# Kernel tuning notes

Hardware: AMD Instinct MI355X
Metric: run time of the kernel (lower is better)

## Reference

```python
import jax, jax.numpy as jnp
import numpy as np

W = 0.5
EM_ITER = 5
SCALE = 20.0
N, T, D_IN, D_OUT, K, C1 = 16, 750, 2048, 2048, 8, 21  # C1 = class_num + 1


def l2n(f):
    # torch.norm(p=2, dim=-1, keepdim=True); divide with 1e-9 eps
    return f / (jnp.linalg.norm(f, axis=-1, keepdims=True) + 1e-9)


def setup_inputs() -> dict:
    key = jax.random.key(0)
    ks = jax.random.split(key, 5)
    x = jax.random.normal(ks[0], (N, T, D_IN), dtype=jnp.float32)
    W_emb = jax.random.normal(ks[1], (D_IN, D_OUT), dtype=jnp.float32) * (1.0 / np.sqrt(D_IN))
    b_emb = jnp.zeros((D_OUT,), dtype=jnp.float32)
    mu_param = jax.random.normal(ks[2], (K, D_OUT), dtype=jnp.float32) * 0.02
    ac_center = jax.random.normal(ks[3], (C1, D_OUT), dtype=jnp.float32) * 0.02
    fg_center = -1.0 * ac_center[-1][None, :]
    return {"x": x, "W_emb": W_emb, "b_emb": b_emb, "mu_param": mu_param,
            "ac_center": ac_center, "fg_center": fg_center}


def em(mu, x):
    norm_x = l2n(x)
    for _ in range(EM_ITER):
        norm_mu = l2n(mu)
        z = jax.nn.softmax(jnp.einsum('nkd,ntd->nkt', norm_mu, norm_x) * 5.0, axis=1)
        nz = z / (jnp.sum(z, axis=-1, keepdims=True) + 1e-9)
        mu = jnp.einsum('nkt,ntd->nkd', nz, x)
    return mu


def random_walk(x, y, w):
    n, t, _ = x.shape
    x_n, y_n = l2n(x), l2n(y)
    z = jax.nn.softmax(jnp.einsum('nkd,ntd->nkt', y_n, x_n) * 5.0, axis=1)  # (n,k,t)
    nz = z / (jnp.sum(z, axis=-1, keepdims=True) + 1e-9)
    affinity = jnp.einsum('nkt,nks->nts', z, nz)                             # (n,t,t)
    eye_t = jnp.eye(t, dtype=x.dtype)
    y2x_sum_x = w * jnp.einsum('nkt,nkd->ntd', z, y) + x
    # (I - w^2 A)^{-1} @ y2x_sum_x, expressed as a batched solve (same math as torch.solve)
    refined = (1.0 - w) * jnp.linalg.solve(eye_t[None] - (w * w) * affinity, y2x_sum_x)
    return refined


def prediction_module(x, ac_center, fg_center):
    nx = l2n(x)
    nac = l2n(ac_center)
    nfg = l2n(fg_center)
    frm_scrs = jnp.einsum('ntd,cd->ntc', nx, nac) * SCALE        # (n,t,C1)
    frm_fb = jnp.einsum('ntd,kd->ntk', nx, nfg)[..., 0] * SCALE  # (n,t)
    ca_att = jax.nn.sigmoid(frm_fb)
    cw_att = jax.nn.sigmoid(frm_scrs)
    ca_natt = ca_att / (jnp.sum(ca_att, axis=1, keepdims=True) + 1e-5)
    cw_natt = cw_att / (jnp.sum(cw_att, axis=1, keepdims=True) + 1e-5)
    ca_feat = jnp.einsum('ntd,nt->nd', x, ca_natt)
    cw_feat = jnp.einsum('ntd,ntc->ncd', x, cw_natt)
    ca_scr = jnp.einsum('nd,cd->nc', l2n(ca_feat), nac) * SCALE
    cw_scr = jnp.einsum('ncd,cd->nc', l2n(cw_feat), nac) * SCALE
    return (jax.nn.softmax(ca_scr, axis=-1), jax.nn.softmax(cw_scr, axis=-1), ca_att, frm_scrs)


def forward(x, W_emb, b_emb, mu_param, ac_center, fg_center):
    n = x.shape[0]
    x = jax.nn.relu(x @ W_emb + b_emb)  # feature_embedding (Dropout is identity in eval)
    mu = jnp.broadcast_to(mu_param[None], (n,) + mu_param.shape)
    mu = em(mu, x)
    reallocated_x = random_walk(x, mu, W)
    o_ca, o_cw, o_att, o_frm = prediction_module(x, ac_center, fg_center)
    m_ca, m_cw, m_att, m_frm = prediction_module(reallocated_x, ac_center, fg_center)
    mu_scr = jnp.einsum('nkd,cd->nkc', l2n(mu), l2n(ac_center)) * SCALE
    mu_pred = jax.nn.softmax(mu_scr, axis=-1)
    return (o_ca, o_cw, o_att, o_frm, m_ca, m_cw, m_att, m_frm, x, mu, mu_pred)


def reference(x, W_emb, b_emb, mu_param, ac_center, fg_center):
    return forward(x, W_emb, b_emb, mu_param, ac_center, fg_center)
```

## Files before the change

kernel.cpp:

```cpp
#include <hip/hip_runtime.h>

#define NB 16
#define TT 750
#define DD 2048
#define KK 8
#define CC 21
#define NT 12000

#define MU_CH 16
#define MU_TCH 47

typedef __bf16 bf16;
typedef __attribute__((ext_vector_type(4))) float floatx4;
typedef __attribute__((ext_vector_type(8))) __bf16 bf16x8;
typedef __attribute__((ext_vector_type(4))) __bf16 bf16x4;

__device__ __forceinline__ float wave_allreduce_sum(float v) {
#pragma unroll
  for (int m = 32; m > 0; m >>= 1) v += __shfl_xor(v, m, 64);
  return v;
}

__device__ __forceinline__ void async_lds16(const bf16* g, bf16* l) {
  __builtin_amdgcn_global_load_lds(
      (const __attribute__((address_space(1))) void*)(g),
      (__attribute__((address_space(3))) void*)(l), 16, 0, 0);
}

__global__ __launch_bounds__(256) void k_prep(
    const float* __restrict__ W, bf16* __restrict__ Wt,
    const float* __restrict__ ac, const float* __restrict__ fg,
    float* __restrict__ nacf, bf16* __restrict__ nacb,
    const float* __restrict__ mup, float* __restrict__ nmu, bf16* __restrict__ nmub,
    const float* __restrict__ x, bf16* __restrict__ Ab) {
  int b = blockIdx.x, tid = threadIdx.x;
  __shared__ float tile[32][33];
  __shared__ float sb[4];
  if (b < 4096) {
    int j0 = (b & 63) * 32, k0 = (b >> 6) * 32;
    int tx = tid & 31, ty = tid >> 5;
#pragma unroll
    for (int i = 0; i < 4; i++)
      tile[ty + 8 * i][tx] = W[(size_t)(k0 + ty + 8 * i) * DD + j0 + tx];
    __syncthreads();
#pragma unroll
    for (int i = 0; i < 4; i++)
      Wt[(size_t)(j0 + ty + 8 * i) * DD + k0 + tx] = (bf16)tile[tx][ty + 8 * i];
    return;
  }
  if (b < 4128) {
    int r = b - 4096;
    int d0 = tid * 8;
    if (r >= 22) {
#pragma unroll
      for (int j = 0; j < 8; j++) nacb[(size_t)r * DD + d0 + j] = (bf16)0.f;
      return;
    }
    const float* src = (r < 21) ? (ac + (size_t)r * DD) : fg;
    float v[8];
    floatx4 a = *(const floatx4*)(src + d0);
    floatx4 c = *(const floatx4*)(src + d0 + 4);
    v[0]=a.x; v[1]=a.y; v[2]=a.z; v[3]=a.w; v[4]=c.x; v[5]=c.y; v[6]=c.z; v[7]=c.w;
    float ss = 0.f;
#pragma unroll
    for (int j = 0; j < 8; j++) ss += v[j] * v[j];
    ss = wave_allreduce_sum(ss);
    int lane = tid & 63, wid = tid >> 6;
    if (lane == 0) sb[wid] = ss;
    __syncthreads();
    float inv = 1.f / (sqrtf(sb[0] + sb[1] + sb[2] + sb[3]) + 1e-9f);
#pragma unroll
    for (int j = 0; j < 8; j++) {
      float nv = v[j] * inv;
      nacf[(size_t)r * DD + d0 + j] = nv;
      nacb[(size_t)r * DD + d0 + j] = (bf16)nv;
    }
    return;
  }
  if (b < 4256) {
    int bb = b - 4128;
    int n = bb >> 3, k = bb & 7;
    int lane = tid & 63, wid = tid >> 6;
    const float* p = mup + (size_t)k * DD + tid * 8;
    float v[8];
    floatx4 a = *(const floatx4*)p;
    floatx4 c = *(const floatx4*)(p + 4);
    v[0]=a.x; v[1]=a.y; v[2]=a.z; v[3]=a.w; v[4]=c.x; v[5]=c.y; v[6]=c.z; v[7]=c.w;
    float ss = 0.f;
#pragma unroll
    for (int j = 0; j < 8; j++) ss += v[j] * v[j];
    ss = wave_allreduce_sum(ss);
    if (lane == 0) sb[wid] = ss;
    __syncthreads();
    float inv = 1.f / (sqrtf(sb[0] + sb[1] + sb[2] + sb[3]) + 1e-9f);
    float* q = nmu + (size_t)bb * DD + tid * 8;
    bf16* qb = nmub + (size_t)(n * 16 + k) * DD + tid * 8;
#pragma unroll
    for (int j = 0; j < 8; j++) {
      float nv = v[j] * inv;
      q[j] = nv;
      qb[j] = (bf16)nv;
    }
    return;
  }
  int unit0 = (b - 4256) * 4;
#pragma unroll
  for (int u = 0; u < 4; u++) {
    size_t base = ((size_t)(unit0 + u) * 256 + tid) * 8;
    int row = (int)(base >> 11);
    bf16x8 o = {};
    if (row < NT) {
      floatx4 a = *(const floatx4*)(x + base);
      floatx4 c = *(const floatx4*)(x + base + 4);
      o[0]=(bf16)a.x; o[1]=(bf16)a.y; o[2]=(bf16)a.z; o[3]=(bf16)a.w;
      o[4]=(bf16)c.x; o[5]=(bf16)c.y; o[6]=(bf16)c.z; o[7]=(bf16)c.w;
    }
    *(bf16x8*)(Ab + base) = o;
  }
}

__global__ __launch_bounds__(256) void k_gemm(
    const bf16* __restrict__ Ab, const bf16* __restrict__ Bt,
    const float* __restrict__ bias,
    float* __restrict__ Cout, bf16* __restrict__ Cb, float* __restrict__ rowsq) {
  __shared__ bf16 As[128 * 64];
  __shared__ bf16 Bs[128 * 64];
  int tid = threadIdx.x;
  int bid = blockIdx.x;
  int xcd = bid & 7;
  int j = bid >> 3;
  int n0 = (xcd * 2 + (j >= 94 ? 1 : 0)) * 128;
  int m0 = (j % 94) * 128;
  int wid = tid >> 6, lane = tid & 63;
  int wm = (wid >> 1) * 64, wn = (wid & 1) * 64;
  int lrow = lane & 15, lko = (lane >> 4) * 8;
  int lr7 = lrow & 7;
  floatx4 acc[4][4] = {};
  int crow = tid >> 3;
  int jg = ((tid & 7) ^ (crow & 7)) * 8;
  const bf16* gA = Ab + (size_t)(m0 + crow) * DD + jg;
  const bf16* gB = Bt + (size_t)(n0 + crow) * DD + jg;
  bf16* lA = As + tid * 8;
  bf16* lB = Bs + tid * 8;
  for (int k0 = 0; k0 < DD; k0 += 64) {
#pragma unroll
    for (int s = 0; s < 4; s++)
      async_lds16(gA + (size_t)(32 * s) * DD + k0, lA + 2048 * s);
#pragma unroll
    for (int s = 0; s < 4; s++)
      async_lds16(gB + (size_t)(32 * s) * DD + k0, lB + 2048 * s);
    __syncthreads();
#pragma unroll
    for (int ks = 0; ks < 64; ks += 32) {
      bf16x8 af[4], bfr[4];
#pragma unroll
      for (int i = 0; i < 4; i++) {
        int sw = (((ks + lko) >> 3) ^ lr7) * 8;
        af[i] = *(const bf16x8*)(As + (wm + i * 16 + lrow) * 64 + sw);
      }
#pragma unroll
      for (int jj = 0; jj < 4; jj++) {
        int sw = (((ks + lko) >> 3) ^ lr7) * 8;
        bfr[jj] = *(const bf16x8*)(Bs + (wn + jj * 16 + lrow) * 64 + sw);
      }
#pragma unroll
      for (int i = 0; i < 4; i++)
#pragma unroll
        for (int jj = 0; jj < 4; jj++)
          acc[i][jj] = __builtin_amdgcn_mfma_f32_16x16x32_bf16(af[i], bfr[jj], acc[i][jj], 0, 0, 0);
    }
    __syncthreads();
  }
  int quad = lane >> 4;
  float bv[4];
#pragma unroll
  for (int jj = 0; jj < 4; jj++) bv[jj] = bias[n0 + wn + jj * 16 + lrow];
#pragma unroll
  for (int i = 0; i < 4; i++) {
#pragma unroll
    for (int r = 0; r < 4; r++) {
      int row = m0 + wm + i * 16 + quad * 4 + r;
      bool ok = (row < NT);
      float sq = 0.f;
#pragma unroll
      for (int jj = 0; jj < 4; jj++) {
        int col = n0 + wn + jj * 16 + lrow;
        float v = acc[i][jj][r] + bv[jj];
        v = fmaxf(v, 0.f);
        if (ok) {
          Cout[(size_t)row * DD + col] = v;
          Cb[(size_t)row * DD + col] = (bf16)v;
        }
        sq += v * v;
      }
#pragma unroll
      for (int m = 1; m < 16; m <<= 1) sq += __shfl_xor(sq, m, 64);
      if (ok && lrow == 0) atomicAdd(&rowsq[row], sq);
    }
  }
}

__global__ __launch_bounds__(256) void k_score(
    const bf16* __restrict__ Xb, const bf16* __restrict__ nmub,
    const float* __restrict__ rowsq,
    float* __restrict__ z, float* __restrict__ rowsum) {
  __shared__ bf16 As[2][64 * 64];
  __shared__ bf16 Bs[2][16 * 64];
  int tid = threadIdx.x, lane = tid & 63, w = tid >> 6;
  int m0 = blockIdx.x * 64, n = blockIdx.y;
  int lrow = lane & 15, lko = (lane >> 4) * 8, lr7 = lrow & 7;
  int crow = tid >> 3;
  int jg = ((tid & 7) ^ (crow & 7)) * 8;
  const bf16* gA = Xb + (size_t)(n * TT + m0 + crow) * DD + jg;
  const bf16* gB = nmub + (size_t)(n * 16 + (crow & 15)) * DD + jg;
  async_lds16(gA, &As[0][tid * 8]);
  async_lds16(gA + (size_t)32 * DD, &As[0][2048 + tid * 8]);
  if (tid < 128) async_lds16(gB, &Bs[0][tid * 8]);
  floatx4 acc = {};
  int buf = 0;
  for (int k0 = 0; k0 < DD; k0 += 64) {
    __syncthreads();
    if (k0 + 64 < DD) {
      async_lds16(gA + k0 + 64, &As[buf ^ 1][tid * 8]);
      async_lds16(gA + (size_t)32 * DD + k0 + 64, &As[buf ^ 1][2048 + tid * 8]);
      if (tid < 128) async_lds16(gB + k0 + 64, &Bs[buf ^ 1][tid * 8]);
    }
#pragma unroll
    for (int ks = 0; ks < 64; ks += 32) {
      int sw = ((((ks + lko) >> 3)) ^ lr7) * 8;
      bf16x8 a = *(const bf16x8*)(&As[buf][(w * 16 + lrow) * 64 + sw]);
      bf16x8 b = *(const bf16x8*)(&Bs[buf][lrow * 64 + sw]);
      acc = __builtin_amdgcn_mfma_f32_16x16x32_bf16(a, b, acc, 0, 0, 0);
    }
    buf ^= 1;
  }
  int quad = lane >> 4;
  int k = lrow;
  float pacc = 0.f;
#pragma unroll
  for (int r = 0; r < 4; r++) {
    int trow = m0 + w * 16 + quad * 4 + r;
    bool valid = (trow < TT);
    float rq = valid ? rowsq[n * TT + trow] : 1.f;
    float s = acc[r] * (5.f / (sqrtf(rq) + 1e-9f));
    float mx = s;
    mx = fmaxf(mx, __shfl_xor(mx, 1, 64));
    mx = fmaxf(mx, __shfl_xor(mx, 2, 64));
    mx = fmaxf(mx, __shfl_xor(mx, 4, 64));
    float e = __expf(s - mx);
    float se = e;
    se += __shfl_xor(se, 1, 64);
    se += __shfl_xor(se, 2, 64);
    se += __shfl_xor(se, 4, 64);
    float zz = e / se;
    zz = (valid && k < 8) ? zz : 0.f;
    if (valid && k < 8) z[(size_t)(n * TT + trow) * 8 + k] = zz;
    pacc += zz;
  }
  pacc += __shfl_xor(pacc, 16, 64);
  pacc += __shfl_xor(pacc, 32, 64);
  if (lane < 8) atomicAdd(&rowsum[n * 8 + lane], pacc);
}

__global__ __launch_bounds__(256) void k_mu_accum(
    const bf16* __restrict__ Xb, const float* __restrict__ z,
    float* __restrict__ part2) {
  int n = blockIdx.x, tc = blockIdx.y, tid = threadIdx.x;
  int t0 = tc * MU_TCH;
  int tcnt = min(MU_TCH, TT - t0);
  __shared__ float zs[MU_TCH * 8];
  for (int i = tid; i < tcnt * 8; i += 256) zs[i] = z[(size_t)(n * TT + t0) * 8 + i];
  __syncthreads();
  float acc[8][8] = {};
  const bf16* xp = Xb + (size_t)(n * TT + t0) * DD + tid * 8;
  bf16x8 x0 = *(const bf16x8*)xp;
  bf16x8 x1 = (tcnt > 1) ? *(const bf16x8*)(xp + DD) : x0;
  for (int tt = 0; tt < tcnt; tt++) {
    bf16x8 cur = x0;
    x0 = x1;
    if (tt + 2 < tcnt) x1 = *(const bf16x8*)(xp + (size_t)(tt + 2) * DD);
    float xv[8];
#pragma unroll
    for (int j = 0; j < 8; j++) xv[j] = (float)cur[j];
    floatx4 za = *(const floatx4*)&zs[tt * 8];
    floatx4 zb4 = *(const floatx4*)&zs[tt * 8 + 4];
    float zk[8] = {za.x, za.y, za.z, za.w, zb4.x, zb4.y, zb4.z, zb4.w};
#pragma unroll
    for (int k = 0; k < 8; k++)
#pragma unroll
      for (int j = 0; j < 8; j++) acc[k][j] += zk[k] * xv[j];
  }
  float* pb = part2 + ((size_t)(tc * 16 + n) * 8) * DD + tid * 8;
#pragma unroll
  for (int k = 0; k < 8; k++) {
    floatx4 lo = {acc[k][0], acc[k][1], acc[k][2], acc[k][3]};
    floatx4 hi = {acc[k][4], acc[k][5], acc[k][6], acc[k][7]};
    *(floatx4*)(pb + (size_t)k * DD) = lo;
    *(floatx4*)(pb + (size_t)k * DD + 4) = hi;
  }
}

__global__ void k_mu_finish(const float* __restrict__ part2, const float* __restrict__ rs,
                            float* __restrict__ accS_raw, float* __restrict__ mu_ws,
                            float* __restrict__ mu_out, float* __restrict__ nmu_out,
                            bf16* __restrict__ nmub) {
  int b = blockIdx.x;
  int n = b >> 3, k = b & 7;
  int tid = threadIdx.x, lane = tid & 63, wid = tid >> 6;
  int d0 = tid * 8;
  float s[8] = {};
#pragma unroll 4
  for (int c = 0; c < MU_CH; c++) {
    const float* p = part2 + ((size_t)(c * 16 + n) * 8 + k) * DD + d0;
    floatx4 a = *(const floatx4*)p;
    floatx4 cc = *(const floatx4*)(p + 4);
    s[0] += a.x; s[1] += a.y; s[2] += a.z; s[3] += a.w;
    s[4] += cc.x; s[5] += cc.y; s[6] += cc.z; s[7] += cc.w;
  }
  if (accS_raw != nullptr) {
#pragma unroll
    for (int j = 0; j < 8; j++) accS_raw[(size_t)b * DD + d0 + j] = s[j];
    return;
  }
  float invr = 1.f / (rs[b] + 1e-9f);
  float m[8];
#pragma unroll
  for (int j = 0; j < 8; j++) m[j] = s[j] * invr;
#pragma unroll
  for (int j = 0; j < 8; j++) mu_ws[(size_t)b * DD + d0 + j] = m[j];
  if (mu_out != nullptr) {
#pragma unroll
    for (int j = 0; j < 8; j++) mu_out[(size_t)b * DD + d0 + j] = m[j];
  }
  float ss = 0.f;
#pragma unroll
  for (int j = 0; j < 8; j++) ss += m[j] * m[j];
  ss = wave_allreduce_sum(ss);
  __shared__ float sb[4];
  if (lane == 0) sb[wid] = ss;
  __syncthreads();
  float inv = 1.f / (sqrtf(sb[0] + sb[1] + sb[2] + sb[3]) + 1e-9f);
  bf16* qb = nmub + (size_t)(n * 16 + k) * DD + d0;
#pragma unroll
  for (int j = 0; j < 8; j++) {
    float nv = m[j] * inv;
    nmu_out[(size_t)b * DD + d0 + j] = nv;
    qb[j] = (bf16)nv;
  }
}

__global__ void k_wood_mupred(const float* __restrict__ z, const float* __restrict__ rowsum,
                              const float* __restrict__ S, const float* __restrict__ mu,
                              float* __restrict__ G,
                              const float* __restrict__ nmu, const float* __restrict__ nacf,
                              float* __restrict__ mupred) {
  int tid = threadIdx.x;
  if (blockIdx.x >= 16) {
    int b = blockIdx.x - 16;
    int lane = tid & 63, wid = tid >> 6;
    const float* v = nmu + (size_t)b * DD;
    __shared__ float scr[21];
    for (int c = wid; c < 21; c += 4) {
      const float* a = nacf + (size_t)c * DD;
      float s = 0.f;
      for (int i = lane * 4; i < DD; i += 256) {
        floatx4 vv = *(const floatx4*)(v + i);
        floatx4 aa = *(const floatx4*)(a + i);
        s += vv.x * aa.x + vv.y * aa.y + vv.z * aa.z + vv.w * aa.w;
      }
      s = wave_allreduce_sum(s);
      if (lane == 0) scr[c] = s * 20.f;
    }
    __syncthreads();
    if (tid == 0) {
      float mx = scr[0];
      for (int c = 1; c < 21; c++) mx = fmaxf(mx, scr[c]);
      float se = 0.f;
      for (int c = 0; c < 21; c++) se += __expf(scr[c] - mx);
      float inv = 1.f / se;
      for (int c = 0; c < 21; c++) mupred[(size_t)b * 21 + c] = __expf(scr[c] - mx) * inv;
    }
    return;
  }
  int n = blockIdx.x;
  __shared__ float VU[8][8];
  __shared__ float Mi[8][8];
  __shared__ float invrs[8];
  __shared__ float vus[64][4];
  if (tid < 8) invrs[tid] = 1.f / (rowsum[n * 8 + tid] + 1e-9f);
  {
    int pr = tid >> 2, sl = tid & 3;
    int jj = pr >> 3, kk = pr & 7;
    float s = 0.f;
    for (int t = sl; t < TT; t += 4) {
      const float* zp = z + (size_t)(n * TT + t) * 8;
      s += zp[jj] * zp[kk];
    }
    vus[pr][sl] = s;
  }
  __syncthreads();
  if (tid < 64)
    VU[tid >> 3][tid & 7] =
        (vus[tid][0] + vus[tid][1] + vus[tid][2] + vus[tid][3]) * invrs[tid >> 3];
  __syncthreads();
  if (tid == 0) {
    float M[8][16];
    for (int i = 0; i < 8; i++)
      for (int jj = 0; jj < 8; jj++) {
        M[i][jj] = ((i == jj) ? 1.f : 0.f) - 0.25f * VU[i][jj];
        M[i][8 + jj] = (i == jj) ? 1.f : 0.f;
      }
    for (int c = 0; c < 8; c++) {
      float pv = 1.f / M[c][c];
      for (int jj = 0; jj < 16; jj++) M[c][jj] *= pv;
      for (int rr = 0; rr < 8; rr++)
        if (rr != c) {
          float f = M[rr][c];
          for (int jj = 0; jj < 16; jj++) M[rr][jj] -= f * M[c][jj];
        }
    }
    for (int i = 0; i < 8; i++)
      for (int jj = 0; jj < 8; jj++) Mi[i][jj] = M[i][8 + jj];
  }
  __syncthreads();
  const float* mun = mu + (size_t)n * 8 * DD;
  const float* Sn = S + (size_t)n * 8 * DD;
  float* Gn = G + (size_t)n * 8 * DD;
  for (int d = tid; d < DD; d += 256) {
    float m[8], P[8];
#pragma unroll
    for (int k = 0; k < 8; k++) m[k] = mun[k * DD + d];
#pragma unroll
    for (int k = 0; k < 8; k++) {
      float s = 0.f;
#pragma unroll
      for (int jj = 0; jj < 8; jj++) s += VU[k][jj] * m[jj];
      P[k] = 0.5f * s + Sn[k * DD + d] * invrs[k];
    }
#pragma unroll
    for (int jj = 0; jj < 8; jj++) {
      float s = 0.f;
#pragma unroll
      for (int k = 0; k < 8; k++) s += Mi[jj][k] * P[k];
      Gn[jj * DD + d] = 0.5f * (0.5f * m[jj] + 0.25f * s);
    }
  }
}

__global__ __launch_bounds__(256) void k_rw_passC(
    const bf16* __restrict__ Xb, const float* __restrict__ z,
    const float* __restrict__ G, bf16* __restrict__ refb,
    float* __restrict__ invr) {
  int n = blockIdx.x, ch = blockIdx.y, tid = threadIdx.x;
  int lane = tid & 63, wid = tid >> 6;
  int d0 = tid * 8;
  int t0 = ch * 30;
  const float* Gn = G + (size_t)n * 8 * DD;
  float gr[8][8];
#pragma unroll
  for (int k = 0; k < 8; k++) {
    floatx4 a = *(const floatx4*)(Gn + k * DD + d0);
    floatx4 b = *(const floatx4*)(Gn + k * DD + d0 + 4);
    gr[k][0]=a.x; gr[k][1]=a.y; gr[k][2]=a.z; gr[k][3]=a.w;
    gr[k][4]=b.x; gr[k][5]=b.y; gr[k][6]=b.z; gr[k][7]=b.w;
  }
  __shared__ float red[30][4];
  const bf16* xrow = Xb + (size_t)n * TT * DD;
  bf16x8 xg = *(const bf16x8*)(xrow + (size_t)t0 * DD + d0);
  for (int tt = 0; tt < 30; tt++) {
    int t = t0 + tt;
    bf16x8 x8 = xg;
    if (tt + 1 < 30) xg = *(const bf16x8*)(xrow + (size_t)(t + 1) * DD + d0);
    const float* zp = z + (size_t)(n * TT + t) * 8;
    floatx4 za = *(const floatx4*)zp;
    floatx4 zb4 = *(const floatx4*)(zp + 4);
    float zt[8] = {za.x, za.y, za.z, za.w, zb4.x, zb4.y, zb4.z, zb4.w};
    float r[8];
#pragma unroll
    for (int j = 0; j < 8; j++) {
      float s = 0.5f * (float)x8[j];
#pragma unroll
      for (int k = 0; k < 8; k++) s += zt[k] * gr[k][j];
      r[j] = s;
    }
    bf16x8 ro;
#pragma unroll
    for (int j = 0; j < 8; j++) ro[j] = (bf16)r[j];
    *(bf16x8*)(refb + (size_t)(n * TT + t) * DD + d0) = ro;
    float ss = 0.f;
#pragma unroll
    for (int j = 0; j < 8; j++) ss += r[j] * r[j];
    ss = wave_allreduce_sum(ss);
    if (lane == 0) red[tt][wid] = ss;
  }
  __syncthreads();
  if (tid < 30) {
    float tot = red[tid][0] + red[tid][1] + red[tid][2] + red[tid][3];
    invr[n * TT + t0 + tid] = 1.f / (sqrtf(tot) + 1e-9f);
  }
}

__global__ __launch_bounds__(256) void k_pred_p1(
    const bf16* __restrict__ Xb, const bf16* __restrict__ nacb,
    const float* __restrict__ invn, int mode,
    float* __restrict__ out_frm, float* __restrict__ out_att,
    float* __restrict__ natt, float* __restrict__ att_sums) {
  __shared__ bf16 As[2][2048];
  __shared__ bf16 Bs[2][2048];
  __shared__ float ssum[2][32];
  int tid = threadIdx.x, lane = tid & 63, wid = tid >> 6;
  int m0 = blockIdx.x * 32;
  if (tid < 64) ssum[tid >> 5][tid & 31] = 0.f;
  int lrow = lane & 15, lko = (lane >> 4) * 8;
  int lr7 = lrow & 7;
  int r0 = (wid & 1) * 16, c0 = (wid >> 1) * 16;
  int crow = tid >> 3;
  int jg = ((tid & 7) ^ (crow & 7)) * 8;
  const bf16* gA = Xb + (size_t)(m0 + crow) * DD + jg;
  const bf16* gB = nacb + (size_t)crow * DD + jg;
  async_lds16(gA, &As[0][tid * 8]);
  async_lds16(gB, &Bs[0][tid * 8]);
  floatx4 acc = {};
  int buf = 0;
  for (int k0 = 0; k0 < DD; k0 += 64) {
    __syncthreads();
    if (k0 + 64 < DD) {
      async_lds16(gA + k0 + 64, &As[buf ^ 1][tid * 8]);
      async_lds16(gB + k0 + 64, &Bs[buf ^ 1][tid * 8]);
    }
#pragma unroll
    for (int ks = 0; ks < 64; ks += 32) {
      int sw = ((((ks + lko) >> 3) ^ lr7)) * 8;
      bf16x8 a = *(const bf16x8*)(&As[buf][(r0 + lrow) * 64 + sw]);
      bf16x8 b = *(const bf16x8*)(&Bs[buf][(c0 + lrow) * 64 + sw]);
      acc = __builtin_amdgcn_mfma_f32_16x16x32_bf16(a, b, acc, 0, 0, 0);
    }
    buf ^= 1;
  }
  __syncthreads();
  int quad = lane >> 4;
  int nbase = m0 / TT;
  int c = c0 + lrow;
#pragma unroll
  for (int r = 0; r < 4; r++) {
    int row = m0 + r0 + quad * 4 + r;
    if (c < 22) {
      float iv = mode ? (1.f / (sqrtf(invn[row]) + 1e-9f)) : invn[row];
      float s = acc[r] * iv * 20.f;
      float sg = 1.f / (1.f + __expf(-s));
      int n_loc = row / TT - nbase;
      if (c < 21) out_frm[(size_t)row * 21 + c] = s;
      else out_att[row] = sg;
      natt[(size_t)row * 22 + c] = sg;
      atomicAdd(&ssum[n_loc][c], sg);
    }
  }
  __syncthreads();
  if (tid < 64) {
    int nl = tid >> 5, cs = tid & 31;
    int nn = nbase + nl;
    if (cs < 22 && nn < NB) {
      float v = ssum[nl][cs];
      if (v != 0.f) atomicAdd(&att_sums[nn * 22 + cs], v);
    }
  }
}

__global__ __launch_bounds__(256) void k_pred_p2(
    const bf16* __restrict__ Xb, const float* __restrict__ natt,
    const float* __restrict__ sums, float* __restrict__ partF) {
  int n = blockIdx.x, dh = blockIdx.y, tc = blockIdx.z, tid = threadIdx.x;
  int d = dh * 1024 + tid * 4;
  int t0 = tc * 94;
  int tcnt = min(94, TT - t0);
  __shared__ float sw[94 * 22];
  for (int i = tid; i < tcnt * 22; i += 256) {
    int c = i - (i / 22) * 22;
    sw[i] = natt[(size_t)(n * TT + t0) * 22 + i] / (sums[n * 22 + c] + 1e-5f);
  }
  __syncthreads();
  float ac[22][4] = {};
  const bf16* xrow = Xb + (size_t)n * TT * DD;
  bf16x4 xg = *(const bf16x4*)(xrow + (size_t)t0 * DD + d);
  for (int tt = 0; tt < tcnt; tt++) {
    bf16x4 x4 = xg;
    if (tt + 1 < tcnt) xg = *(const bf16x4*)(xrow + (size_t)(t0 + tt + 1) * DD + d);
    float xv[4] = {(float)x4[0], (float)x4[1], (float)x4[2], (float)x4[3]};
#pragma unroll
    for (int cidx = 0; cidx < 22; cidx++) {
      float w = sw[tt * 22 + cidx];
#pragma unroll
      for (int jj = 0; jj < 4; jj++) ac[cidx][jj] += w * xv[jj];
    }
  }
  float* pb = partF + ((size_t)(n * 8 + tc) * 22) * DD + d;
#pragma unroll
  for (int cidx = 0; cidx < 22; cidx++) {
    floatx4 v = {ac[cidx][0], ac[cidx][1], ac[cidx][2], ac[cidx][3]};
    *(floatx4*)(pb + (size_t)cidx * DD) = v;
  }
}

__global__ void k_feat_finish(const float* __restrict__ partF, float* __restrict__ feats) {
  int idx = blockIdx.x * 256 + threadIdx.x;
  if (idx >= NB * 22 * DD) return;
  int n = idx / (22 * DD);
  int rem = idx - n * (22 * DD);
  const float* p = partF + ((size_t)n * 8) * (22 * DD) + rem;
  float s = 0.f;
#pragma unroll
  for (int tc = 0; tc < 8; tc++) s += p[(size_t)tc * 22 * DD];
  feats[idx] = s;
}

__global__ void k_pred_final(const float* __restrict__ feats, const float* __restrict__ nacf,
                             float* __restrict__ oca, float* __restrict__ ocw) {
  int n = blockIdx.x, tid = threadIdx.x, lane = tid & 63, wid = tid >> 6;
  const float* fn = feats + (size_t)n * 22 * DD;
  __shared__ float rnorm[22];
  __shared__ float scr[42];
  for (int r = wid; r < 22; r += 4) {
    const float* fv = fn + (size_t)r * DD;
    float s = 0.f;
    for (int i = lane * 4; i < DD; i += 256) {
      floatx4 v = *(const floatx4*)(fv + i);
      s += v.x * v.x + v.y * v.y + v.z * v.z + v.w * v.w;
    }
    s = wave_allreduce_sum(s);
    if (lane == 0) rnorm[r] = 1.f / (sqrtf(s) + 1e-9f);
  }
  __syncthreads();
  for (int idx = wid; idx < 42; idx += 4) {
    int c = (idx < 21) ? idx : (idx - 21);
    int fr = (idx < 21) ? c : 21;
    const float* fv = fn + (size_t)fr * DD;
    const float* av = nacf + (size_t)c * DD;
    float s = 0.f;
    for (int i = lane * 4; i < DD; i += 256) {
      floatx4 v = *(const floatx4*)(fv + i);
      floatx4 a = *(const floatx4*)(av + i);
      s += v.x * a.x + v.y * a.y + v.z * a.z + v.w * a.w;
    }
    s = wave_allreduce_sum(s);
    if (lane == 0) scr[idx] = s * 20.f * rnorm[fr];
  }
  __syncthreads();
  if (tid < 2) {
    int base = (tid == 0) ? 21 : 0;
    float* dst = ((tid == 0) ? oca : ocw) + (size_t)n * 21;
    float mx = scr[base];
    for (int c = 1; c < 21; c++) mx = fmaxf(mx, scr[base + c]);
    float se = 0.f;
    for (int c = 0; c < 21; c++) se += __expf(scr[base + c] - mx);
    float inv = 1.f / se;
    for (int c = 0; c < 21; c++) dst[c] = __expf(scr[base + c] - mx) * inv;
  }
}

extern "C" void kernel_launch(void* const* d_in, const int* in_sizes, int n_in,
                              void* d_out, int out_size, void* d_ws, size_t ws_size,
                              hipStream_t stream) {
  const float* x_in = (const float*)d_in[0];
  const float* W = (const float*)d_in[1];
  const float* bemb = (const float*)d_in[2];
  const float* mup = (const float*)d_in[3];
  const float* ac = (const float*)d_in[4];
  const float* fg = (const float*)d_in[5];
  float* out = (float*)d_out;

  char* ws = (char*)d_ws;
  bf16* Wt = (bf16*)ws;
  bf16* Xb = (bf16*)(ws + 8388608);
  bf16* Rb = (bf16*)(ws + 57671680);
  bf16* Ab = (bf16*)(ws + 106954752);
  float* part2 = (float*)(ws + 106954752);
  float* partF = (float*)(ws + 106954752);
  bf16* nacb = (bf16*)(ws + 156237824);
  float* f = (float*)(ws + 156368896);
  float* nacf = f;
  float* mu = nacf + 45056;
  float* nmu = mu + 262144;
  bf16* nmub = (bf16*)(nmu + 262144);
  float* accS = nmu + 262144 + 262144;
  float* G = accS + 262144;
  float* z = G + 262144;
  float* natt = z + 96000;
  float* feats = natt + 264000;
  float* invr = feats + 720896;
  float* rowsum = invr + 12032;
  float* asums_o = rowsum + 768;
  float* asums_m = asums_o + 352;
  float* rowsq = asums_m + 352;

  float* o_ca = out;
  float* o_cw = out + 336;
  float* o_att = out + 672;
  float* o_frm = out + 12672;
  float* m_ca = out + 264672;
  float* m_cw = out + 265008;
  float* m_att = out + 265344;
  float* m_frm = out + 277344;
  float* x_out = out + 529344;
  float* mu_out = out + 25105344;
  float* mup_out = out + 25367488;

  hipMemsetAsync(rowsum, 0, (768 + 352 + 352 + 12032) * sizeof(float), stream);
  hipMemsetAsync(nmub, 0, (size_t)NB * 16 * DD * sizeof(bf16), stream);
  k_prep<<<7264, 256, 0, stream>>>(W, Wt, ac, fg, nacf, nacb, mup, nmu, nmub, x_in, Ab);
  k_gemm<<<1504, 256, 0, stream>>>(Ab, Wt, bemb, x_out, Xb, rowsq);
  for (int it = 0; it < 5; it++) {
    bool last = (it == 4);
    k_score<<<dim3(12, 16), 256, 0, stream>>>(Xb, nmub, rowsq, z, rowsum + it * 128);
    k_mu_accum<<<dim3(16, MU_CH), 256, 0, stream>>>(Xb, z, part2);
    k_mu_finish<<<128, 256, 0, stream>>>(part2, rowsum + it * 128, nullptr, mu,
                                         last ? mu_out : nullptr, nmu, nmub);
  }
  k_score<<<dim3(12, 16), 256, 0, stream>>>(Xb, nmub, rowsq, z, rowsum + 5 * 128);
  k_mu_accum<<<dim3(16, MU_CH), 256, 0, stream>>>(Xb, z, part2);
  k_mu_finish<<<128, 256, 0, stream>>>(part2, nullptr, accS, nullptr, nullptr, nullptr, nullptr);
  k_wood_mupred<<<144, 256, 0, stream>>>(z, rowsum + 5 * 128, accS, mu, G, nmu, nacf, mup_out);
  k_rw_passC<<<dim3(16, 25), 256, 0, stream>>>(Xb, z, G, Rb, invr);
  k_pred_p1<<<375, 256, 0, stream>>>(Xb, nacb, rowsq, 1, o_frm, o_att, natt, asums_o);
  k_pred_p2<<<dim3(16, 2, 8), 256, 0, stream>>>(Xb, natt, asums_o, partF);
  k_feat_finish<<<2816, 256, 0, stream>>>(partF, feats);
  k_pred_final<<<16, 256, 0, stream>>>(feats, nacf, o_ca, o_cw);
  k_pred_p1<<<375, 256, 0, stream>>>(Rb, nacb, invr, 0, m_frm, m_att, natt, asums_m);
  k_pred_p2<<<dim3(16, 2, 8), 256, 0, stream>>>(Rb, natt, asums_m, partF);
  k_feat_finish<<<2816, 256, 0, stream>>>(partF, feats);
  k_pred_final<<<16, 256, 0, stream>>>(feats, nacf, m_ca, m_cw);
}
```

Before: 915.9 us.

## Widen K-tile to 256 in score and pred GEMMs; fuse feat reduction into pred_final

The k_score and k_pred_p1 GEMM loops now stage 256-wide K slices in shared memory instead of 64, with a matching XOR swizzle. This cuts the number of barriers and loop iterations by four and issues more async loads per phase, at the cost of much larger LDS per block (about 80KB for k_score), which may lower occupancy. Separately, the k_feat_finish reduction over the 8 t-chunks is folded into k_pred_final, removing one launch per prediction pass. The cost is that this reduction now runs on only 16 blocks.

New measurement: 889.0 us. 1.03x faster.

```diff
diff --git a/kernel.cpp b/kernel.cpp
--- a/kernel.cpp
+++ b/kernel.cpp
@@ -204,32 +204,54 @@
     const bf16* __restrict__ Xb, const bf16* __restrict__ nmub,
     const float* __restrict__ rowsq,
     float* __restrict__ z, float* __restrict__ rowsum) {
-  __shared__ bf16 As[2][64 * 64];
-  __shared__ bf16 Bs[2][16 * 64];
+  __shared__ bf16 As[2][64 * 256];
+  __shared__ bf16 Bs[2][16 * 256];
   int tid = threadIdx.x, lane = tid & 63, w = tid >> 6;
   int m0 = blockIdx.x * 64, n = blockIdx.y;
   int lrow = lane & 15, lko = (lane >> 4) * 8, lr7 = lrow & 7;
-  int crow = tid >> 3;
-  int jg = ((tid & 7) ^ (crow & 7)) * 8;
-  const bf16* gA = Xb + (size_t)(n * TT + m0 + crow) * DD + jg;
-  const bf16* gB = nmub + (size_t)(n * 16 + (crow & 15)) * DD + jg;
-  async_lds16(gA, &As[0][tid * 8]);
-  async_lds16(gA + (size_t)32 * DD, &As[0][2048 + tid * 8]);
-  if (tid < 128) async_lds16(gB, &Bs[0][tid * 8]);
+  int scg = tid & 31;
+  int srow = tid >> 5;
+  const bf16* gXn = Xb + (size_t)(n * TT + m0) * DD;
+  const bf16* gBn = nmub + (size_t)(n * 16) * DD;
+#pragma unroll
+  for (int r = 0; r < 8; r++) {
+    int row = r * 8 + srow;
+    int cgg = (scg & 24) | ((scg & 7) ^ (row & 7));
+    async_lds16(gXn + (size_t)row * DD + cgg * 8, &As[0][r * 2048 + tid * 8]);
+  }
+#pragma unroll
+  for (int r = 0; r < 2; r++) {
+    int row = r * 8 + srow;
+    int cgg = (scg & 24) | ((scg & 7) ^ (row & 7));
+    async_lds16(gBn + (size_t)row * DD + cgg * 8, &Bs[0][r * 2048 + tid * 8]);
+  }
   floatx4 acc = {};
   int buf = 0;
-  for (int k0 = 0; k0 < DD; k0 += 64) {
+  for (int k0 = 0; k0 < DD; k0 += 256) {
     __syncthreads();
-    if (k0 + 64 < DD) {
-      async_lds16(gA + k0 + 64, &As[buf ^ 1][tid * 8]);
-      async_lds16(gA + (size_t)32 * DD + k0 + 64, &As[buf ^ 1][2048 + tid * 8]);
-      if (tid < 128) async_lds16(gB + k0 + 64, &Bs[buf ^ 1][tid * 8]);
-    }
-#pragma unroll
-    for (int ks = 0; ks < 64; ks += 32) {
-      int sw = ((((ks + lko) >> 3)) ^ lr7) * 8;
-      bf16x8 a = *(const bf16x8*)(&As[buf][(w * 16 + lrow) * 64 + sw]);
-      bf16x8 b = *(const bf16x8*)(&Bs[buf][lrow * 64 + sw]);
+    if (k0 + 256 < DD) {
+#pragma unroll
+      for (int r = 0; r < 8; r++) {
+        int row = r * 8 + srow;
+        int cgg = (scg & 24) | ((scg & 7) ^ (row & 7));
+        async_lds16(gXn + (size_t)row * DD + k0 + 256 + cgg * 8,
+                    &As[buf ^ 1][r * 2048 + tid * 8]);
+      }
+#pragma unroll
+      for (int r = 0; r < 2; r++) {
+        int row = r * 8 + srow;
+        int cgg = (scg & 24) | ((scg & 7) ^ (row & 7));
+        async_lds16(gBn + (size_t)row * DD + k0 + 256 + cgg * 8,
+                    &Bs[buf ^ 1][r * 2048 + tid * 8]);
+      }
+    }
+    int arow = w * 16 + lrow;
+#pragma unroll
+    for (int ks = 0; ks < 256; ks += 32) {
+      int cg = (ks + lko) >> 3;
+      int cgl = (cg & 24) | ((cg & 7) ^ lr7);
+      bf16x8 a = *(const bf16x8*)(&As[buf][arow * 256 + cgl * 8]);
+      bf16x8 b = *(const bf16x8*)(&Bs[buf][lrow * 256 + cgl * 8]);
       acc = __builtin_amdgcn_mfma_f32_16x16x32_bf16(a, b, acc, 0, 0, 0);
     }
     buf ^= 1;
@@ -505,34 +527,46 @@
     const float* __restrict__ invn, int mode,
     float* __restrict__ out_frm, float* __restrict__ out_att,
     float* __restrict__ natt, float* __restrict__ att_sums) {
-  __shared__ bf16 As[2][2048];
-  __shared__ bf16 Bs[2][2048];
+  __shared__ bf16 As[2][32 * 256];
+  __shared__ bf16 Bs[2][32 * 256];
   __shared__ float ssum[2][32];
   int tid = threadIdx.x, lane = tid & 63, wid = tid >> 6;
   int m0 = blockIdx.x * 32;
   if (tid < 64) ssum[tid >> 5][tid & 31] = 0.f;
-  int lrow = lane & 15, lko = (lane >> 4) * 8;
-  int lr7 = lrow & 7;
+  int lrow = lane & 15, lko = (lane >> 4) * 8, lr7 = lrow & 7;
   int r0 = (wid & 1) * 16, c0 = (wid >> 1) * 16;
-  int crow = tid >> 3;
-  int jg = ((tid & 7) ^ (crow & 7)) * 8;
-  const bf16* gA = Xb + (size_t)(m0 + crow) * DD + jg;
-  const bf16* gB = nacb + (size_t)crow * DD + jg;
-  async_lds16(gA, &As[0][tid * 8]);
-  async_lds16(gB, &Bs[0][tid * 8]);
+  int scg = tid & 31;
+  int srow = tid >> 5;
+  const bf16* gA = Xb + (size_t)m0 * DD;
+  const bf16* gB = nacb;
+#pragma unroll
+  for (int r = 0; r < 4; r++) {
+    int row = r * 8 + srow;
+    int cgg = (scg & 24) | ((scg & 7) ^ (row & 7));
+    async_lds16(gA + (size_t)row * DD + cgg * 8, &As[0][r * 2048 + tid * 8]);
+    async_lds16(gB + (size_t)row * DD + cgg * 8, &Bs[0][r * 2048 + tid * 8]);
+  }
   floatx4 acc = {};
   int buf = 0;
-  for (int k0 = 0; k0 < DD; k0 += 64) {
+  for (int k0 = 0; k0 < DD; k0 += 256) {
     __syncthreads();
-    if (k0 + 64 < DD) {
-      async_lds16(gA + k0 + 64, &As[buf ^ 1][tid * 8]);
-      async_lds16(gB + k0 + 64, &Bs[buf ^ 1][tid * 8]);
-    }
-#pragma unroll
-    for (int ks = 0; ks < 64; ks += 32) {
-      int sw = ((((ks + lko) >> 3) ^ lr7)) * 8;
-      bf16x8 a = *(const bf16x8*)(&As[buf][(r0 + lrow) * 64 + sw]);
-      bf16x8 b = *(const bf16x8*)(&Bs[buf][(c0 + lrow) * 64 + sw]);
+    if (k0 + 256 < DD) {
+#pragma unroll
+      for (int r = 0; r < 4; r++) {
+        int row = r * 8 + srow;
+        int cgg = (scg & 24) | ((scg & 7) ^ (row & 7));
+        async_lds16(gA + (size_t)row * DD + k0 + 256 + cgg * 8,
+                    &As[buf ^ 1][r * 2048 + tid * 8]);
+        async_lds16(gB + (size_t)row * DD + k0 + 256 + cgg * 8,
+                    &Bs[buf ^ 1][r * 2048 + tid * 8]);
+      }
+    }
+#pragma unroll
+    for (int ks = 0; ks < 256; ks += 32) {
+      int cg = (ks + lko) >> 3;
+      int cgl = (cg & 24) | ((cg & 7) ^ lr7);
+      bf16x8 a = *(const bf16x8*)(&As[buf][(r0 + lrow) * 256 + cgl * 8]);
+      bf16x8 b = *(const bf16x8*)(&Bs[buf][(c0 + lrow) * 256 + cgl * 8]);
       acc = __builtin_amdgcn_mfma_f32_16x16x32_bf16(a, b, acc, 0, 0, 0);
     }
     buf ^= 1;
@@ -601,22 +635,24 @@
   }
 }
 
-__global__ void k_feat_finish(const float* __restrict__ partF, float* __restrict__ feats) {
-  int idx = blockIdx.x * 256 + threadIdx.x;
-  if (idx >= NB * 22 * DD) return;
-  int n = idx / (22 * DD);
-  int rem = idx - n * (22 * DD);
-  const float* p = partF + ((size_t)n * 8) * (22 * DD) + rem;
-  float s = 0.f;
-#pragma unroll
-  for (int tc = 0; tc < 8; tc++) s += p[(size_t)tc * 22 * DD];
-  feats[idx] = s;
-}
-
-__global__ void k_pred_final(const float* __restrict__ feats, const float* __restrict__ nacf,
+__global__ void k_pred_final(const float* __restrict__ partF, float* __restrict__ feats,
+                             const float* __restrict__ nacf,
                              float* __restrict__ oca, float* __restrict__ ocw) {
   int n = blockIdx.x, tid = threadIdx.x, lane = tid & 63, wid = tid >> 6;
-  const float* fn = feats + (size_t)n * 22 * DD;
+  float* fnw = feats + (size_t)n * 22 * DD;
+  const float* pp = partF + ((size_t)n * 8) * (22 * DD);
+  for (int i = tid * 4; i < 22 * DD; i += 1024) {
+    floatx4 s = {};
+#pragma unroll
+    for (int tc = 0; tc < 8; tc++) {
+      floatx4 v = *(const floatx4*)(pp + (size_t)tc * 22 * DD + i);
+      s.x += v.x; s.y += v.y; s.z += v.z; s.w += v.w;
+    }
+    *(floatx4*)(fnw + i) = s;
+  }
+  __threadfence_block();
+  __syncthreads();
+  const float* fn = fnw;
   __shared__ float rnorm[22];
   __shared__ float scr[42];
   for (int r = wid; r < 22; r += 4) {
@@ -722,10 +758,8 @@
   k_rw_passC<<<dim3(16, 25), 256, 0, stream>>>(Xb, z, G, Rb, invr);
   k_pred_p1<<<375, 256, 0, stream>>>(Xb, nacb, rowsq, 1, o_frm, o_att, natt, asums_o);
   k_pred_p2<<<dim3(16, 2, 8), 256, 0, stream>>>(Xb, natt, asums_o, partF);
-  k_feat_finish<<<2816, 256, 0, stream>>>(partF, feats);
-  k_pred_final<<<16, 256, 0, stream>>>(feats, nacf, o_ca, o_cw);
+  k_pred_final<<<16, 256, 0, stream>>>(partF, feats, nacf, o_ca, o_cw);
   k_pred_p1<<<375, 256, 0, stream>>>(Rb, nacb, invr, 0, m_frm, m_att, natt, asums_m);
   k_pred_p2<<<dim3(16, 2, 8), 256, 0, stream>>>(Rb, natt, asums_m, partF);
-  k_feat_finish<<<2816, 256, 0, stream>>>(partF, feats);
-  k_pred_final<<<16, 256, 0, stream>>>(feats, nacf, m_ca, m_cw);
-}
+  k_pred_final<<<16, 256, 0, stream>>>(partF, feats, nacf, m_ca, m_cw);
+}
```
